# Performance work log

Hardware: AMD Instinct MI355X
Metric: run time of the kernel (lower is better)

The kernel has to match this reference:

```python
import jax, jax.numpy as jnp
import numpy as np

BS = 16384
NUM_ALLY, NUM_ADV, NUM_LM = 3, 2, 3
ALLY_D, ADV_D, LM_D = 4, 4, 2
HEAD, HID, HYPER = 4, 64, 64
OUT = HEAD * HID  # 256


def _lin_init(key, fan_in, fan_out):
    k1, k2 = jax.random.split(key)
    s = 1.0 / np.sqrt(fan_in)
    W = jax.random.uniform(k1, (fan_in, fan_out), minval=-s, maxval=s, dtype=jnp.float32)
    b = jax.random.uniform(k2, (fan_out,), minval=-s, maxval=s, dtype=jnp.float32)
    return W, b


def setup_inputs() -> dict:
    key = jax.random.key(0)
    ks = jax.random.split(key, 12)
    inputs = jax.random.normal(ks[0], (BS, 30), dtype=jnp.float32)
    hidden_state = jnp.zeros((1, HID), dtype=jnp.float32)
    actions = jax.random.normal(ks[1], (BS, 2), dtype=jnp.float32)
    self_W, self_b = _lin_init(ks[2], 4, HID)
    ally_W1, ally_b1 = _lin_init(ks[3], ALLY_D, HYPER)
    ally_W2, ally_b2 = _lin_init(ks[4], HYPER, (ALLY_D + 1) * OUT)
    adv_W1, adv_b1 = _lin_init(ks[5], ADV_D, HYPER)
    adv_W2, adv_b2 = _lin_init(ks[6], HYPER, (ADV_D + 1) * OUT)
    lm_W1, lm_b1 = _lin_init(ks[7], LM_D, HYPER)
    lm_W2, lm_b2 = _lin_init(ks[8], HYPER, (LM_D + 1) * OUT)
    merger_w = jnp.ones((1, HEAD, HID), dtype=jnp.float32)
    fc1_W, fc1_b = _lin_init(ks[9], HID + 2, HID)
    fc2_W, fc2_b = _lin_init(ks[10], HID, 1)
    return dict(inputs=inputs, hidden_state=hidden_state, actions=actions,
                self_W=self_W, self_b=self_b,
                ally_W1=ally_W1, ally_b1=ally_b1, ally_W2=ally_W2, ally_b2=ally_b2,
                adv_W1=adv_W1, adv_b1=adv_b1, adv_W2=adv_W2, adv_b2=adv_b2,
                lm_W1=lm_W1, lm_b1=lm_b1, lm_W2=lm_W2, lm_b2=lm_b2,
                merger_w=merger_w, fc1_W=fc1_W, fc1_b=fc1_b, fc2_W=fc2_W, fc2_b=fc2_b)


def _split_obs(ob):
    self_feats = ob[:, :4]
    i1 = 4 + NUM_LM * LM_D
    lm = ob[:, 4:i1].reshape(-1, NUM_LM, LM_D)
    i2 = i1 + NUM_ALLY * 2
    ally_pos = ob[:, i1:i2].reshape(-1, NUM_ALLY, 2)
    i3 = i2 + NUM_ADV * 2
    adv_pos = ob[:, i2:i3].reshape(-1, NUM_ADV, 2)
    i4 = i3 + NUM_ALLY * 2
    ally_vel = ob[:, i3:i4].reshape(-1, NUM_ALLY, 2)
    i5 = i4 + NUM_ADV * 2
    adv_vel = ob[:, i4:i5].reshape(-1, NUM_ADV, 2)
    ally = jnp.concatenate([ally_pos, ally_vel], axis=-1)
    adv = jnp.concatenate([adv_pos, adv_vel], axis=-1)
    return self_feats, ally, adv, lm


def _branch(feats, W1, b1, W2, b2, d, n):
    # feats: [bs, n, d] -> per-entity hypernet weight [d, HEAD*HID] and bias
    h = jax.nn.leaky_relu(feats @ W1 + b1, negative_slope=0.01)
    out = h @ W2 + b2                              # [bs, n, (d+1)*256]
    w = out[..., :d * OUT].reshape(-1, d, OUT)     # [bs*n, d, 256]
    b = out[..., d * OUT:].reshape(-1, 1, OUT)     # [bs*n, 1, 256]
    y = jnp.matmul(feats.reshape(-1, 1, d), w) + b # [bs*n, 1, 256]
    return y.reshape(-1, n, HEAD, HID).sum(axis=1) # [bs, HEAD, HID]


def reference(inputs, hidden_state, actions,
              self_W, self_b,
              ally_W1, ally_b1, ally_W2, ally_b2,
              adv_W1, adv_b1, adv_W2, adv_b2,
              lm_W1, lm_b1, lm_W2, lm_b2,
              merger_w, fc1_W, fc1_b, fc2_W, fc2_b):
    self_feats, ally_feats, adv_feats, lm_feats = _split_obs(inputs)
    self_out = self_feats @ self_W + self_b                       # [bs, 64]
    ally_out = _branch(ally_feats, ally_W1, ally_b1, ally_W2, ally_b2, ALLY_D, NUM_ALLY)
    adv_out = _branch(adv_feats, adv_W1, adv_b1, adv_W2, adv_b2, ADV_D, NUM_ADV)
    lm_out = _branch(lm_feats, lm_W1, lm_b1, lm_W2, lm_b2, LM_D, NUM_LM)
    tmp = ally_out + lm_out + adv_out                             # [bs, 4, 64]
    merged = jnp.sum(jax.nn.softmax(merger_w, axis=1) * tmp, axis=1)
    out = jax.nn.relu(self_out + merged)
    out = jnp.concatenate([out, actions.reshape(-1, actions.shape[-1])], axis=-1)
    x = jax.nn.relu(out @ fc1_W + fc1_b)
    q = x @ fc2_W + fc2_b
    return q, x
```

## Files before the change

kernel.cpp:

```cpp
#include <hip/hip_runtime.h>

typedef __attribute__((ext_vector_type(8))) _Float16 f16x8;
typedef __attribute__((ext_vector_type(4))) float f32x4;

#define KTOT 864
#define FSTRIDE 872
#define OSTRIDE 104

__global__ __launch_bounds__(256) void precompute_kernel(
    const float* __restrict__ selfW, const float* __restrict__ selfB,
    const float* __restrict__ W2a, const float* __restrict__ b2a,
    const float* __restrict__ W2d, const float* __restrict__ b2d,
    const float* __restrict__ W2l, const float* __restrict__ b2l,
    const float* __restrict__ mergerW,
    const float* __restrict__ fc1W, const float* __restrict__ fc1b,
    _Float16* __restrict__ matB, _Float16* __restrict__ fc1B)
{
  int g = blockIdx.x * 256 + threadIdx.x;
  if (g < 64 * KTOT) {
    int j8 = g & 7;
    int l  = (g >> 3) & 63;
    int t  = g >> 9;
    int nt = t & 3, kk = t >> 2;
    int c  = nt * 16 + (l & 15);
    int k  = kk * 32 + (l >> 4) * 8 + j8;

    float v0 = mergerW[c], v1 = mergerW[64 + c], v2 = mergerW[128 + c], v3 = mergerW[192 + c];
    float mx = fmaxf(fmaxf(v0, v1), fmaxf(v2, v3));
    float e0 = expf(v0 - mx), e1 = expf(v1 - mx), e2 = expf(v2 - mx), e3 = expf(v3 - mx);
    float inv = 1.f / (e0 + e1 + e2 + e3);
    float w0 = e0 * inv, w1 = e1 * inv, w2 = e2 * inv, w3 = e3 * inv;
    auto HS = [&](const float* __restrict__ p, int base) -> float {
      return w0 * p[base + c] + w1 * p[base + 64 + c] + w2 * p[base + 128 + c] + w3 * p[base + 192 + c];
    };
    float val = 0.f;
    if (k < 256)      { int j = k >> 2, kkk = k & 3;              val = HS(W2a, j * 1280 + kkk * 256); }
    else if (k < 320) { int j = k - 256;                          val = HS(W2a, j * 1280 + 1024); }
    else if (k < 324) { int kkk = k - 320;                        val = HS(b2a, kkk * 256); }
    else if (k < 580) { int k2 = k - 324; int j = k2 >> 2, kkk = k2 & 3; val = HS(W2d, j * 1280 + kkk * 256); }
    else if (k < 644) { int j = k - 580;                          val = HS(W2d, j * 1280 + 1024); }
    else if (k < 648) { int kkk = k - 644;                        val = HS(b2d, kkk * 256); }
    else if (k < 776) { int k2 = k - 648; int j = k2 >> 1, kkk = k2 & 1; val = HS(W2l, j * 768 + kkk * 256); }
    else if (k < 840) { int j = k - 776;                          val = HS(W2l, j * 768 + 512); }
    else if (k < 842) { int kkk = k - 840;                        val = HS(b2l, kkk * 256); }
    else if (k < 846) {                                           val = selfW[(k - 842) * 64 + c]; }
    else if (k == 846){ val = 3.f * HS(b2a, 1024) + 2.f * HS(b2d, 1024) + 3.f * HS(b2l, 512) + selfB[c]; }
    matB[g] = (_Float16)val;
  } else {
    int g2 = g - 64 * KTOT;
    int j8 = g2 & 7;
    int l  = (g2 >> 3) & 63;
    int t  = g2 >> 9;
    int nt = t & 3, kk = t >> 2;
    int c  = nt * 16 + (l & 15);
    int k  = kk * 32 + (l >> 4) * 8 + j8;
    float val = 0.f;
    if (k < 66)       val = fc1W[k * 64 + c];
    else if (k == 66) val = fc1b[c];
    fc1B[g2] = (_Float16)val;
  }
}

__global__ __launch_bounds__(128) void hpn_main(
    const float* __restrict__ inputs, const float* __restrict__ actions,
    const float* __restrict__ W1a, const float* __restrict__ B1a,
    const float* __restrict__ W1d, const float* __restrict__ B1d,
    const float* __restrict__ W1l, const float* __restrict__ B1l,
    const _Float16* __restrict__ matB, const _Float16* __restrict__ fc1B,
    const float* __restrict__ fc2W, const float* __restrict__ fc2b,
    float* __restrict__ q_out, float* __restrict__ x_out)
{
  __shared__ __align__(16) float    stage[16 * 32];
  __shared__ __align__(16) _Float16 feats[16 * FSTRIDE];
  __shared__ __align__(16) _Float16 outact[16 * OSTRIDE];
  __shared__ __align__(16) float    partial[64 * 16];

  const int tid  = threadIdx.x;
  const int lane = tid & 63;
  const int wave = tid >> 6;
  const int base = blockIdx.x * 16;
  const int m = lane & 15;
  const int quad = lane >> 4;

  float sbuf[4];
#pragma unroll
  for (int c = 0; c < 4; ++c) {
    int idx = lane + c * 64;
    int row = wave * 8 + (idx >> 5), col = idx & 31;
    sbuf[c] = (col < 30) ? inputs[(base + row) * 30 + col] : 0.f;
  }
  float a0 = 0.f, a1 = 0.f;
  if (tid < 16) { a0 = actions[base * 2 + 2 * tid]; a1 = actions[base * 2 + 2 * tid + 1]; }

  float w1a0 = W1a[lane], w1a1 = W1a[64 + lane], w1a2 = W1a[128 + lane], w1a3 = W1a[192 + lane];
  float vb1a = B1a[lane];
  float w1d0 = W1d[lane], w1d1 = W1d[64 + lane], w1d2 = W1d[128 + lane], w1d3 = W1d[192 + lane];
  float vb1d = B1d[lane];
  float w1l0 = W1l[lane], w1l1 = W1l[64 + lane];
  float vb1l = B1l[lane];

  float wq0 = fc2W[m], wq1 = fc2W[16 + m], wq2 = fc2W[32 + m], wq3 = fc2W[48 + m];
  float qb = fc2b[0];

  const _Float16* bbase = matB + lane * 8;
  const int kk0 = wave * 13;
  f16x8 bp[4];
#pragma unroll
  for (int nt = 0; nt < 4; ++nt) bp[nt] = *(const f16x8*)(bbase + (kk0 * 4 + nt) * 512);

#pragma unroll
  for (int c = 0; c < 4; ++c) {
    int idx = lane + c * 64;
    int row = wave * 8 + (idx >> 5), col = idx & 31;
    stage[row * 32 + col] = sbuf[c];
  }
#pragma unroll
  for (int p = 0; p < 2; ++p) {
    int idx = p * 64 + lane;
    int row = wave * 8 + (idx >> 4), d = idx & 15;
    *(float*)(feats + row * FSTRIDE + 832 + d * 2) = 0.f;
  }
#pragma unroll
  for (int p = 0; p < 2; ++p) {
    int idx = p * 128 + tid;
    int row = idx >> 4, d = idx & 15;
    *(float*)(outact + row * OSTRIDE + 64 + d * 2) = 0.f;
  }

  for (int ii = 0; ii < 8; ++ii) {
    int i = wave * 8 + ii;
    float r[30];
#pragma unroll
    for (int e = 0; e < 30; ++e) r[e] = stage[i * 32 + e];
    _Float16* fr = feats + i * FSTRIDE;

    float Ua0 = 0, Ua1 = 0, Ua2 = 0, Ua3 = 0, hsa = 0;
#pragma unroll
    for (int n = 0; n < 3; ++n) {
      float f0 = r[10 + 2 * n], f1 = r[11 + 2 * n];
      float f2 = r[20 + 2 * n], f3 = r[21 + 2 * n];
      float t = fmaf(f0, w1a0, fmaf(f1, w1a1, fmaf(f2, w1a2, fmaf(f3, w1a3, vb1a))));
      float h = t > 0.f ? t : 0.01f * t;
      Ua0 = fmaf(h, f0, Ua0); Ua1 = fmaf(h, f1, Ua1);
      Ua2 = fmaf(h, f2, Ua2); Ua3 = fmaf(h, f3, Ua3); hsa += h;
    }
    {
      auto p0 = __builtin_amdgcn_cvt_pkrtz(Ua0, Ua1);
      auto p1 = __builtin_amdgcn_cvt_pkrtz(Ua2, Ua3);
      *(decltype(p0)*)(fr + 4 * lane) = p0;
      *(decltype(p1)*)(fr + 4 * lane + 2) = p1;
      fr[256 + lane] = (_Float16)hsa;
    }

    float Ud0 = 0, Ud1 = 0, Ud2 = 0, Ud3 = 0, hsd = 0;
#pragma unroll
    for (int n = 0; n < 2; ++n) {
      float f0 = r[16 + 2 * n], f1 = r[17 + 2 * n];
      float f2 = r[26 + 2 * n], f3 = r[27 + 2 * n];
      float t = fmaf(f0, w1d0, fmaf(f1, w1d1, fmaf(f2, w1d2, fmaf(f3, w1d3, vb1d))));
      float h = t > 0.f ? t : 0.01f * t;
      Ud0 = fmaf(h, f0, Ud0); Ud1 = fmaf(h, f1, Ud1);
      Ud2 = fmaf(h, f2, Ud2); Ud3 = fmaf(h, f3, Ud3); hsd += h;
    }
    {
      auto p0 = __builtin_amdgcn_cvt_pkrtz(Ud0, Ud1);
      auto p1 = __builtin_amdgcn_cvt_pkrtz(Ud2, Ud3);
      *(decltype(p0)*)(fr + 324 + 4 * lane) = p0;
      *(decltype(p1)*)(fr + 324 + 4 * lane + 2) = p1;
      fr[580 + lane] = (_Float16)hsd;
    }

    float Ul0 = 0, Ul1 = 0, hsl = 0;
#pragma unroll
    for (int n = 0; n < 3; ++n) {
      float f0 = r[4 + 2 * n], f1 = r[5 + 2 * n];
      float t = fmaf(f0, w1l0, fmaf(f1, w1l1, vb1l));
      float h = t > 0.f ? t : 0.01f * t;
      Ul0 = fmaf(h, f0, Ul0); Ul1 = fmaf(h, f1, Ul1); hsl += h;
    }
    {
      auto pl = __builtin_amdgcn_cvt_pkrtz(Ul0, Ul1);
      *(decltype(pl)*)(fr + 648 + 2 * lane) = pl;
      fr[776 + lane] = (_Float16)hsl;
    }
  }

#pragma unroll
  for (int p = 0; p < 2; ++p) {
    int idx = p * 64 + lane;
    int i = wave * 8 + (idx >> 4), t = idx & 15;
    const float* rs = stage + i * 32;
    float val;
    if (t < 4)       { int b = ((t < 2) ? 10 : 20) + (t & 1); val = rs[b] + rs[b + 2] + rs[b + 4]; }
    else if (t < 8)  { int b = ((t < 6) ? 16 : 26) + (t & 1); val = rs[b] + rs[b + 2]; }
    else if (t < 10) { int b = 4 + (t & 1);                   val = rs[b] + rs[b + 2] + rs[b + 4]; }
    else if (t < 14) {                                        val = rs[t - 10]; }
    else if (t == 14){                                        val = 1.0f; }
    else             {                                        val = 0.0f; }
    int k = (t < 4) ? 320 + t : (t < 8) ? 640 + t : (t < 15) ? 832 + t : 863;
    feats[i * FSTRIDE + k] = (_Float16)val;
  }

  __syncthreads();

  f32x4 acc[4];
#pragma unroll
  for (int nt = 0; nt < 4; ++nt) acc[nt] = (f32x4){0.f, 0.f, 0.f, 0.f};

  const _Float16* aptr = feats + m * FSTRIDE + quad * 8;
  {
    f16x8 af = *(const f16x8*)(aptr + kk0 * 32);
#pragma unroll
    for (int nt = 0; nt < 4; ++nt)
      acc[nt] = __builtin_amdgcn_mfma_f32_16x16x32_f16(af, bp[nt], acc[nt], 0, 0, 0);
  }
  const int kkend = kk0 + 13 + wave;
#pragma unroll 3
  for (int kk = kk0 + 1; kk < kkend; ++kk) {
    f16x8 af = *(const f16x8*)(aptr + kk * 32);
#pragma unroll
    for (int nt = 0; nt < 4; ++nt) {
      f16x8 bf = *(const f16x8*)(bbase + (kk * 4 + nt) * 512);
      acc[nt] = __builtin_amdgcn_mfma_f32_16x16x32_f16(af, bf, acc[nt], 0, 0, 0);
    }
  }

  if (wave == 1) {
#pragma unroll
    for (int nt = 0; nt < 4; ++nt)
#pragma unroll
      for (int i = 0; i < 4; ++i)
        partial[(nt * 4 + i) * 64 + lane] = acc[nt][i];
  }
  __syncthreads();
  if (wave == 1) return;
#pragma unroll
  for (int nt = 0; nt < 4; ++nt)
#pragma unroll
    for (int i = 0; i < 4; ++i)
      acc[nt][i] += partial[(nt * 4 + i) * 64 + lane];

  const _Float16* cbase = fc1B + lane * 8;
  f16x8 cfrag[12];
#pragma unroll
  for (int t = 0; t < 12; ++t) cfrag[t] = *(const f16x8*)(cbase + t * 512);

#pragma unroll
  for (int nt = 0; nt < 4; ++nt)
#pragma unroll
    for (int i = 0; i < 4; ++i) {
      int rrow = quad * 4 + i;
      float v = fmaxf(acc[nt][i], 0.f);
      outact[rrow * OSTRIDE + nt * 16 + m] = (_Float16)v;
    }
  if (lane < 16) {
    _Float16* orp = outact + lane * OSTRIDE;
    orp[64] = (_Float16)a0;
    orp[65] = (_Float16)a1;
    orp[66] = (_Float16)1.0f;
  }

  f32x4 xacc[4];
#pragma unroll
  for (int nt = 0; nt < 4; ++nt) xacc[nt] = (f32x4){0.f, 0.f, 0.f, 0.f};
  const _Float16* aptr2 = outact + m * OSTRIDE + quad * 8;
#pragma unroll
  for (int kk = 0; kk < 3; ++kk) {
    f16x8 af = *(const f16x8*)(aptr2 + kk * 32);
#pragma unroll
    for (int nt = 0; nt < 4; ++nt)
      xacc[nt] = __builtin_amdgcn_mfma_f32_16x16x32_f16(af, cfrag[kk * 4 + nt], xacc[nt], 0, 0, 0);
  }

#pragma unroll
  for (int i = 0; i < 4; ++i) {
    int rrow = quad * 4 + i;
    int s = base + rrow;
    float x0 = fmaxf(xacc[0][i], 0.f);
    float x1 = fmaxf(xacc[1][i], 0.f);
    float x2 = fmaxf(xacc[2][i], 0.f);
    float x3 = fmaxf(xacc[3][i], 0.f);
    x_out[s * 64 + m]      = x0;
    x_out[s * 64 + 16 + m] = x1;
    x_out[s * 64 + 32 + m] = x2;
    x_out[s * 64 + 48 + m] = x3;
    float p = fmaf(x0, wq0, fmaf(x1, wq1, fmaf(x2, wq2, x3 * wq3)));
    p += __shfl_xor(p, 1, 64);
    p += __shfl_xor(p, 2, 64);
    p += __shfl_xor(p, 4, 64);
    p += __shfl_xor(p, 8, 64);
    if (m == 0) q_out[s] = p + qb;
  }
}

extern "C" void kernel_launch(void* const* d_in, const int* in_sizes, int n_in,
                              void* d_out, int out_size, void* d_ws, size_t ws_size,
                              hipStream_t stream) {
  const float* inputs  = (const float*)d_in[0];
  const float* actions = (const float*)d_in[2];
  const float* selfW   = (const float*)d_in[3];
  const float* selfB   = (const float*)d_in[4];
  const float* W1a = (const float*)d_in[5],  *B1a = (const float*)d_in[6];
  const float* W2a = (const float*)d_in[7],  *b2a = (const float*)d_in[8];
  const float* W1d = (const float*)d_in[9],  *B1d = (const float*)d_in[10];
  const float* W2d = (const float*)d_in[11], *b2d = (const float*)d_in[12];
  const float* W1l = (const float*)d_in[13], *B1l = (const float*)d_in[14];
  const float* W2l = (const float*)d_in[15], *b2l = (const float*)d_in[16];
  const float* mergerW = (const float*)d_in[17];
  const float* fc1W = (const float*)d_in[18], *fc1b = (const float*)d_in[19];
  const float* fc2W = (const float*)d_in[20], *fc2b = (const float*)d_in[21];

  _Float16* matB = (_Float16*)d_ws;
  _Float16* fc1B = matB + 64 * KTOT;

  const int n = in_sizes[0] / 30;
  precompute_kernel<<<240, 256, 0, stream>>>(selfW, selfB, W2a, b2a, W2d, b2d,
                                             W2l, b2l, mergerW, fc1W, fc1b,
                                             matB, fc1B);
  float* q_out = (float*)d_out;
  float* x_out = q_out + n;
  hpn_main<<<n / 16, 128, 0, stream>>>(inputs, actions, W1a, B1a, W1d, B1d,
                                       W1l, B1l, matB, fc1B, fc2W, fc2b,
                                       q_out, x_out);
}
```

Baseline: 109.1 us.

## Process 32 rows per block with four waves splitting K and reusing B fragments

Each block now handles 32 samples using 256 threads. Each of the four waves covers a quarter of the K dimension and computes two 16-row M tiles, so every B fragment loaded from global memory is reused twice. Partial sums from all waves go through shared memory that aliases the feats buffer, and stage/outact share a second region to keep LDS use low. Two waves then reduce the partials and run fc1/fc2. The cost is an extra barrier, a four-way LDS reduction, and half the waves sitting idle during the tail.

```diff
diff --git a/kernel.cpp b/kernel.cpp
--- a/kernel.cpp
+++ b/kernel.cpp
@@ -61,7 +61,7 @@
   }
 }
 
-__global__ __launch_bounds__(128) void hpn_main(
+__global__ __launch_bounds__(256) void hpn_main(
     const float* __restrict__ inputs, const float* __restrict__ actions,
     const float* __restrict__ W1a, const float* __restrict__ B1a,
     const float* __restrict__ W1d, const float* __restrict__ B1d,
@@ -70,15 +70,17 @@
     const float* __restrict__ fc2W, const float* __restrict__ fc2b,
     float* __restrict__ q_out, float* __restrict__ x_out)
 {
-  __shared__ __align__(16) float    stage[16 * 32];
-  __shared__ __align__(16) _Float16 feats[16 * FSTRIDE];
-  __shared__ __align__(16) _Float16 outact[16 * OSTRIDE];
-  __shared__ __align__(16) float    partial[64 * 16];
+  __shared__ __align__(16) _Float16 feats[32 * FSTRIDE];
+  __shared__ __align__(16) char     regionB[32 * OSTRIDE * 2];
+
+  float*    stage  = (float*)regionB;
+  _Float16* outact = (_Float16*)regionB;
+  float*    partial = (float*)feats;
 
   const int tid  = threadIdx.x;
   const int lane = tid & 63;
   const int wave = tid >> 6;
-  const int base = blockIdx.x * 16;
+  const int base = blockIdx.x * 32;
   const int m = lane & 15;
   const int quad = lane >> 4;
 
@@ -90,7 +92,10 @@
     sbuf[c] = (col < 30) ? inputs[(base + row) * 30 + col] : 0.f;
   }
   float a0 = 0.f, a1 = 0.f;
-  if (tid < 16) { a0 = actions[base * 2 + 2 * tid]; a1 = actions[base * 2 + 2 * tid + 1]; }
+  if (wave < 2 && lane < 16) {
+    int s = base + wave * 16 + lane;
+    a0 = actions[2 * s]; a1 = actions[2 * s + 1];
+  }
 
   float w1a0 = W1a[lane], w1a1 = W1a[64 + lane], w1a2 = W1a[128 + lane], w1a3 = W1a[192 + lane];
   float vb1a = B1a[lane];
@@ -103,7 +108,8 @@
   float qb = fc2b[0];
 
   const _Float16* bbase = matB + lane * 8;
-  const int kk0 = wave * 13;
+  const int kk0 = wave * 7;
+  const int cnt = (wave == 3) ? 6 : 7;
   f16x8 bp[4];
 #pragma unroll
   for (int nt = 0; nt < 4; ++nt) bp[nt] = *(const f16x8*)(bbase + (kk0 * 4 + nt) * 512);
@@ -119,12 +125,6 @@
     int idx = p * 64 + lane;
     int row = wave * 8 + (idx >> 4), d = idx & 15;
     *(float*)(feats + row * FSTRIDE + 832 + d * 2) = 0.f;
-  }
-#pragma unroll
-  for (int p = 0; p < 2; ++p) {
-    int idx = p * 128 + tid;
-    int row = idx >> 4, d = idx & 15;
-    *(float*)(outact + row * OSTRIDE + 64 + d * 2) = 0.f;
   }
 
   for (int ii = 0; ii < 8; ++ii) {
@@ -203,58 +203,76 @@
 
   __syncthreads();
 
-  f32x4 acc[4];
-#pragma unroll
-  for (int nt = 0; nt < 4; ++nt) acc[nt] = (f32x4){0.f, 0.f, 0.f, 0.f};
-
-  const _Float16* aptr = feats + m * FSTRIDE + quad * 8;
+  f32x4 acc0[4], acc1[4];
+#pragma unroll
+  for (int nt = 0; nt < 4; ++nt) { acc0[nt] = (f32x4){0,0,0,0}; acc1[nt] = (f32x4){0,0,0,0}; }
+
+  const _Float16* aptr0 = feats + m * FSTRIDE + quad * 8;
+  const _Float16* aptr1 = feats + (16 + m) * FSTRIDE + quad * 8;
   {
-    f16x8 af = *(const f16x8*)(aptr + kk0 * 32);
-#pragma unroll
-    for (int nt = 0; nt < 4; ++nt)
-      acc[nt] = __builtin_amdgcn_mfma_f32_16x16x32_f16(af, bp[nt], acc[nt], 0, 0, 0);
-  }
-  const int kkend = kk0 + 13 + wave;
+    f16x8 af0 = *(const f16x8*)(aptr0 + kk0 * 32);
+    f16x8 af1 = *(const f16x8*)(aptr1 + kk0 * 32);
+#pragma unroll
+    for (int nt = 0; nt < 4; ++nt) {
+      acc0[nt] = __builtin_amdgcn_mfma_f32_16x16x32_f16(af0, bp[nt], acc0[nt], 0, 0, 0);
+      acc1[nt] = __builtin_amdgcn_mfma_f32_16x16x32_f16(af1, bp[nt], acc1[nt], 0, 0, 0);
+    }
+  }
 #pragma unroll 3
-  for (int kk = kk0 + 1; kk < kkend; ++kk) {
-    f16x8 af = *(const f16x8*)(aptr + kk * 32);
+  for (int kk = kk0 + 1; kk < kk0 + cnt; ++kk) {
+    f16x8 af0 = *(const f16x8*)(aptr0 + kk * 32);
+    f16x8 af1 = *(const f16x8*)(aptr1 + kk * 32);
 #pragma unroll
     for (int nt = 0; nt < 4; ++nt) {
       f16x8 bf = *(const f16x8*)(bbase + (kk * 4 + nt) * 512);
-      acc[nt] = __builtin_amdgcn_mfma_f32_16x16x32_f16(af, bf, acc[nt], 0, 0, 0);
-    }
-  }
-
-  if (wave == 1) {
-#pragma unroll
-    for (int nt = 0; nt < 4; ++nt)
-#pragma unroll
-      for (int i = 0; i < 4; ++i)
-        partial[(nt * 4 + i) * 64 + lane] = acc[nt][i];
-  }
+      acc0[nt] = __builtin_amdgcn_mfma_f32_16x16x32_f16(af0, bf, acc0[nt], 0, 0, 0);
+      acc1[nt] = __builtin_amdgcn_mfma_f32_16x16x32_f16(af1, bf, acc1[nt], 0, 0, 0);
+    }
+  }
+
   __syncthreads();
-  if (wave == 1) return;
+
 #pragma unroll
   for (int nt = 0; nt < 4; ++nt)
 #pragma unroll
-    for (int i = 0; i < 4; ++i)
-      acc[nt][i] += partial[(nt * 4 + i) * 64 + lane];
+    for (int i = 0; i < 4; ++i) {
+      partial[((wave * 2 + 0) * 16 + nt * 4 + i) * 64 + lane] = acc0[nt][i];
+      partial[((wave * 2 + 1) * 16 + nt * 4 + i) * 64 + lane] = acc1[nt][i];
+    }
+  __syncthreads();
+  if (wave >= 2) return;
 
   const _Float16* cbase = fc1B + lane * 8;
   f16x8 cfrag[12];
 #pragma unroll
   for (int t = 0; t < 12; ++t) cfrag[t] = *(const f16x8*)(cbase + t * 512);
 
+  float facc[16];
+#pragma unroll
+  for (int g = 0; g < 16; ++g) {
+    facc[g] = partial[((0 * 2 + wave) * 16 + g) * 64 + lane]
+            + partial[((1 * 2 + wave) * 16 + g) * 64 + lane]
+            + partial[((2 * 2 + wave) * 16 + g) * 64 + lane]
+            + partial[((3 * 2 + wave) * 16 + g) * 64 + lane];
+  }
+
+  const int rbase = wave * 16;
+#pragma unroll
+  for (int p = 0; p < 4; ++p) {
+    int idx = p * 64 + lane;
+    int row = rbase + (idx >> 4), d = idx & 15;
+    *(float*)(outact + row * OSTRIDE + 64 + d * 2) = 0.f;
+  }
 #pragma unroll
   for (int nt = 0; nt < 4; ++nt)
 #pragma unroll
     for (int i = 0; i < 4; ++i) {
-      int rrow = quad * 4 + i;
-      float v = fmaxf(acc[nt][i], 0.f);
+      int rrow = rbase + quad * 4 + i;
+      float v = fmaxf(facc[nt * 4 + i], 0.f);
       outact[rrow * OSTRIDE + nt * 16 + m] = (_Float16)v;
     }
   if (lane < 16) {
-    _Float16* orp = outact + lane * OSTRIDE;
+    _Float16* orp = outact + (rbase + lane) * OSTRIDE;
     orp[64] = (_Float16)a0;
     orp[65] = (_Float16)a1;
     orp[66] = (_Float16)1.0f;
@@ -262,8 +280,8 @@
 
   f32x4 xacc[4];
 #pragma unroll
-  for (int nt = 0; nt < 4; ++nt) xacc[nt] = (f32x4){0.f, 0.f, 0.f, 0.f};
-  const _Float16* aptr2 = outact + m * OSTRIDE + quad * 8;
+  for (int nt = 0; nt < 4; ++nt) xacc[nt] = (f32x4){0,0,0,0};
+  const _Float16* aptr2 = outact + (rbase + m) * OSTRIDE + quad * 8;
 #pragma unroll
   for (int kk = 0; kk < 3; ++kk) {
     f16x8 af = *(const f16x8*)(aptr2 + kk * 32);
@@ -274,8 +292,7 @@
 
 #pragma unroll
   for (int i = 0; i < 4; ++i) {
-    int rrow = quad * 4 + i;
-    int s = base + rrow;
+    int s = base + rbase + quad * 4 + i;
     float x0 = fmaxf(xacc[0][i], 0.f);
     float x1 = fmaxf(xacc[1][i], 0.f);
     float x2 = fmaxf(xacc[2][i], 0.f);
@@ -319,7 +336,7 @@
                                              matB, fc1B);
   float* q_out = (float*)d_out;
   float* x_out = q_out + n;
-  hpn_main<<<n / 16, 128, 0, stream>>>(inputs, actions, W1a, B1a, W1d, B1d,
+  hpn_main<<<n / 32, 256, 0, stream>>>(inputs, actions, W1a, B1a, W1d, B1d,
                                        W1l, B1l, matB, fc1B, fc2W, fc2b,
                                        q_out, x_out);
 }
```

After: 107.2 us. No clear change (-1.8%).
